# Optimization experiments

Hardware: AMD Instinct MI355X
Metric: run time of the kernel (lower is better)

## Reference

```python
import jax, jax.numpy as jnp
from jax import lax
import numpy as np

N = 4096      # nnodes
D = 64        # embed_dim
R = 128       # nodes per region
G = N // R    # 32 regions (contiguous blocks)
BIG = 1e9     # 'no edge' cost (scipy MST treats zero-similarity entries as absent edges)


def setup_inputs() -> dict:
    key = jax.random.key(0)
    emb = jax.random.normal(key, (N, D), dtype=jnp.float32) * 0.05  # nn.Embedding weight (xavier-like scale)
    region_id = jnp.arange(N) // R
    inter_mask = (region_id[:, None] != region_id[None, :]).astype(jnp.float32)  # block off-diagonal buffer
    return {"emb_weight": emb, "inter_mask": inter_mask, "inter_budget": 1024}


def _prim_forest_mask(W):
    """Prim's algorithm on dense cost matrix W [R,R] (BIG = missing edge).
    Returns symmetric 0/1 minimum-spanning-FOREST edge mask, matching
    scipy.sparse.csgraph.minimum_spanning_tree on the same graph (weights distinct)."""
    r = W.shape[0]

    def step(carry, _):
        in_tree, key_, parent, mask = carry
        km = jnp.where(in_tree, BIG, key_)
        u = jnp.argmin(km)                          # cheapest node to attach
        valid = (km[u] < BIG * 0.5).astype(W.dtype)  # BIG key => start new component, no edge
        p = parent[u]
        mask = mask.at[u, p].add(valid)
        mask = mask.at[p, u].add(valid)
        in_tree = in_tree.at[u].set(True)
        wu = W[u]
        improve = (~in_tree) & (wu < key_)
        key_ = jnp.where(improve, wu, key_)
        parent = jnp.where(improve, u, parent)
        return (in_tree, key_, parent, mask), None

    in_tree0 = jnp.zeros(r, dtype=bool).at[0].set(True)
    key0 = W[0]
    parent0 = jnp.zeros(r, dtype=jnp.int32)
    mask0 = jnp.zeros_like(W)
    (_, _, _, mask), _ = lax.scan(step, (in_tree0, key0, parent0, mask0), None, length=r - 1)
    return (mask > 0).astype(W.dtype)


def reference(emb_weight, inter_mask, inter_budget):
    # adj_dense = relu(tanh(E E^T))  [N,N]
    adj = jax.nn.relu(jnp.tanh(emb_weight @ emb_weight.T))
    adj_ng = lax.stop_gradient(adj)  # torch: MST input is .detach(); top-k indices carry no grad

    # ---- intra: per-region MST (max spanning forest of similarity == min SF of -sim) ----
    blocks = adj_ng.reshape(G, R, G, R)[jnp.arange(G), :, jnp.arange(G), :]  # [G,R,R] diagonal blocks
    eye = jnp.eye(R, dtype=bool)
    W = jnp.where((blocks > 0) & ~eye, -blocks, BIG)  # zero similarity => no edge (scipy semantics)
    intra_blocks = jax.vmap(_prim_forest_mask)(W)     # [G,R,R]
    idx = jnp.arange(N).reshape(G, R)
    intra = jnp.zeros((N, N), adj.dtype).at[idx[:, :, None], idx[:, None, :]].set(intra_blocks)
    intra = intra * (1.0 - jnp.eye(N, dtype=adj.dtype))  # fill_diagonal_(0)

    # ---- inter: global top-k over upper-triangular masked similarities ----
    flat = jnp.triu(adj_ng * inter_mask, k=1).reshape(-1)  # [N*N]
    k = int(inter_budget)  # == min(budget, nnz(inter_mask)//2); budget is smaller by construction
    _, top_idx = lax.top_k(flat, k)
    inter_sel = jnp.zeros(N * N, adj.dtype).at[top_idx].set(1.0).reshape(N, N)
    inter_sel = inter_sel + inter_sel.T

    final_mask = ((intra + inter_sel) > 0).astype(adj.dtype)
    return adj * final_mask
```

## Files before the change

kernel.cpp:

```cpp
#include <hip/hip_runtime.h>

#define NN 4096
#define DD 64
#define RR 128
#define GG 32
constexpr unsigned BIGH = 0xCE6E6B28u;
constexpr unsigned FLOOR_KEY = 0x3D000000u;
constexpr int FLOORB = 0x3D0;
constexpr int NBINS  = 64;
constexpr unsigned POISON = 0xAAAAAAAAu;

constexpr int WS_FH   = 0;
constexpr int WS_ECNT = 2051;
constexpr int WS_CCNT = 2052;
constexpr int WS_MIJ  = 2112;
constexpr int WS_MV   = WS_MIJ + 4096;
constexpr int WS_EI   = WS_MV + 4096;
constexpr int WS_EJ   = WS_EI + 8192;
constexpr int WS_EV   = WS_EJ + 8192;
constexpr int WS_CK   = WS_EV + 8192;
constexpr int WS_CI   = WS_CK + 8192;
constexpr int EDGE_CAP = 8192;
constexpr int CAND_CAP = 8192;

__device__ __forceinline__ void pair_decode(int p, int& gi, int& gj) {
  gi = 0;
  int rem = p;
  while (rem >= GG - 1 - gi) { rem -= GG - 1 - gi; ++gi; }
  gj = gi + 1 + rem;
}

__device__ __forceinline__ void scan_bins(const unsigned* __restrict__ ws, unsigned k,
                                          unsigned* shm ,
                                          unsigned& tlo, unsigned& thi, unsigned& rem) {
  const int t = threadIdx.x;
  if (t < NBINS) shm[t] = ws[WS_FH + FLOORB + t] - POISON;
  __syncthreads();
  if (t == 0) {
    unsigned cum = 0;
    int fb = FLOORB;
    unsigned r = 0;
    for (int b = NBINS - 1; b >= 0; --b) {
      unsigned c = shm[b];
      if (cum + c >= k) { fb = FLOORB + b; r = k - cum; break; }
      cum += c;
    }
    shm[64] = ((unsigned)fb) << 20;
    shm[65] = ((unsigned)(fb + 1)) << 20;
    shm[66] = r;
  }
  __syncthreads();
  tlo = shm[64];
  thi = shm[65];
  rem = shm[66];
}

__global__ __launch_bounds__(256) void gemm_adj_kernel(const float* __restrict__ E,
                                                       float* __restrict__ adj,
                                                       unsigned* __restrict__ ws) {
  const int ti = blockIdx.y, tj = blockIdx.x;
  const bool rdiag = (ti >> 1) == (tj >> 1);
  if (tj < ti && !rdiag) return;
  const bool cross = (tj >> 1) > (ti >> 1);

  __shared__ float4 As4[64 * 16];
  __shared__ float4 Bs4[64 * 16];
  __shared__ unsigned h[NBINS];
  const float4* E4 = (const float4*)E;
  const int bi = ti * 64, bj = tj * 64;
  const int tid = threadIdx.x;

  if (tid < NBINS) h[tid] = 0;

#pragma unroll
  for (int it = 0; it < 4; ++it) {
    int row = (tid >> 4) + it * 16;
    int g = tid & 15;
    int sw = g ^ ((row >> 2) & 7);
    As4[row * 16 + sw] = E4[(bi + row) * 16 + g];
    Bs4[row * 16 + sw] = E4[(bj + row) * 16 + g];
  }
  __syncthreads();

  const int i0 = (tid >> 4) * 4;
  const int j0 = (tid & 15) * 4;
  const int sa = (i0 >> 2) & 7;
  const int sb = (j0 >> 2) & 7;
  float acc[4][4] = {};
#pragma unroll 2
  for (int k4 = 0; k4 < 16; ++k4) {
    float4 av[4], bv[4];
#pragma unroll
    for (int r = 0; r < 4; ++r) av[r] = As4[(i0 + r) * 16 + (k4 ^ sa)];
#pragma unroll
    for (int c = 0; c < 4; ++c) bv[c] = Bs4[(j0 + c) * 16 + (k4 ^ sb)];
#pragma unroll
    for (int r = 0; r < 4; ++r)
#pragma unroll
      for (int c = 0; c < 4; ++c) {
        acc[r][c] += av[r].x * bv[c].x;
        acc[r][c] += av[r].y * bv[c].y;
        acc[r][c] += av[r].z * bv[c].z;
        acc[r][c] += av[r].w * bv[c].w;
      }
  }
#pragma unroll
  for (int r = 0; r < 4; ++r) {
    float4 o;
    float* p = &o.x;
#pragma unroll
    for (int c = 0; c < 4; ++c) {
      float t = tanhf(acc[r][c]);
      p[c] = t > 0.f ? t : 0.f;
    }
    *(float4*)(adj + (size_t)(bi + i0 + r) * NN + bj + j0) = o;
    if (cross) {
#pragma unroll
      for (int c = 0; c < 4; ++c) {
        unsigned key = __float_as_uint(p[c]);
        if (key >= FLOOR_KEY) atomicAdd(&h[(key >> 20) - FLOORB], 1u);
      }
    }
  }
  if (cross) {
    __syncthreads();
    if (tid < NBINS) {
      unsigned c = h[tid];
      if (c) atomicAdd(&ws[WS_FH + FLOORB + tid], c);
    }
  }
}

template <int CTRL>
__device__ __forceinline__ unsigned dpp_umin(unsigned v) {
  unsigned o = (unsigned)__builtin_amdgcn_update_dpp((int)v, (int)v, CTRL, 0xF, 0xF, false);
  return o < v ? o : v;
}
__device__ __forceinline__ unsigned xfneg(float a) {
  return ~__float_as_uint(a) & 0x7FFFFFFFu;
}

__global__ __launch_bounds__(64) void mst_kernel(const float* __restrict__ adj, unsigned* ws) {
  __shared__ float W[RR * RR];
  const int g = blockIdx.x, l = threadIdx.x, base = g * RR;
  float4* W4 = (float4*)W;
  const float4* A4 = (const float4*)adj;

#pragma unroll
  for (int n = 0; n < 64; ++n) {
    int f = l + 64 * n;
    W4[f] = A4[(size_t)(base + (f >> 5)) * (NN / 4) + (base >> 2) + (f & 31)];
  }
  __syncthreads();

  const int n0 = l, n1 = l + 64;
  float a0 = W[n0], a1 = W[n1];
  unsigned key0 = (n0 != 0 && a0 > 0.f) ? xfneg(a0) : BIGH;
  unsigned key1 = (a1 > 0.f) ? xfneg(a1) : BIGH;
  bool in0 = (l == 0), in1 = false;
  int par0 = 0, par1 = 0;
  unsigned e0ij = 0xFFFFFFFFu, e1ij = 0xFFFFFFFFu;
  float e0v = 0.f, e1v = 0.f;

  for (int it = 0; it < RR - 1; ++it) {
    const unsigned kA = in0 ? BIGH : key0;
    const unsigned kB = in1 ? BIGH : key1;
    unsigned km = kA < kB ? kA : kB;
    km = dpp_umin<0xB1>(km);
    km = dpp_umin<0x4E>(km);
    km = dpp_umin<0x141>(km);
    km = dpp_umin<0x140>(km);
    const unsigned r0 = (unsigned)__builtin_amdgcn_readlane((int)km, 15);
    const unsigned r1 = (unsigned)__builtin_amdgcn_readlane((int)km, 31);
    const unsigned r2 = (unsigned)__builtin_amdgcn_readlane((int)km, 47);
    const unsigned r3 = (unsigned)__builtin_amdgcn_readlane((int)km, 63);
    const unsigned ma = r0 < r1 ? r0 : r1;
    const unsigned mb = r2 < r3 ? r2 : r3;
    const unsigned m = ma < mb ? ma : mb;

    const unsigned long long b0 = __ballot(kA == m);
    const unsigned long long b1 = __ballot(kB == m);
    const int u = b0 ? (__ffsll((unsigned long long)b0) - 1)
                     : (64 + __ffsll((unsigned long long)b1) - 1);

    const int p0 = __builtin_amdgcn_readlane(par0, u & 63);
    const int p1 = __builtin_amdgcn_readlane(par1, u & 63);
    const int par = (u >> 6) ? p1 : p0;
    unsigned pij = 0xFFFFFFFFu;
    float pv = 0.f;
    if ((int)m >= 0) {
      pij = ((unsigned)(base + u) << 12) | (unsigned)(base + par);
      pv = __uint_as_float(~m & 0x7FFFFFFFu);
    }
    const bool mine = (l == (it & 63));
    if (it & 64) { if (mine) { e1ij = pij; e1v = pv; } }
    else         { if (mine) { e0ij = pij; e0v = pv; } }

    in0 = in0 || (u == n0);
    in1 = in1 || (u == n1);
    float w0v = W[u * RR + n0];
    float w1v = W[u * RR + n1];
    unsigned w0 = (w0v > 0.f && n0 != u) ? xfneg(w0v) : BIGH;
    unsigned w1 = (w1v > 0.f && n1 != u) ? xfneg(w1v) : BIGH;
    if (!in0 && w0 < key0) { key0 = w0; par0 = u; }
    if (!in1 && w1 < key1) { key1 = w1; par1 = u; }
  }
  ws[WS_MIJ + base + l] = e0ij;
  ws[WS_MIJ + base + 64 + l] = e1ij;
  ((float*)(ws + WS_MV))[base + l] = e0v;
  ((float*)(ws + WS_MV))[base + 64 + l] = e1v;
}

__global__ __launch_bounds__(256) void collect_kernel(const float* __restrict__ adj,
                                                      unsigned* ws, const int* budget) {
  __shared__ unsigned shm[67];
  unsigned tlo, thi, rem;
  scan_bins(ws, (unsigned)budget[0], shm, tlo, thi, rem);
  (void)rem;
  int gi, gj;
  pair_decode(blockIdx.x, gi, gj);
  const float4* a4 = (const float4*)adj;
  for (int e = threadIdx.x; e < RR * 32; e += 256) {
    int r = e >> 5, c4 = e & 31;
    float4 v = a4[(size_t)(gi * RR + r) * (NN / 4) + gj * 32 + c4];
    float comp[4] = {v.x, v.y, v.z, v.w};
#pragma unroll
    for (int c = 0; c < 4; ++c) {
      float x = comp[c];
      if (!(x > 0.f)) continue;
      unsigned key = __float_as_uint(x);
      if (key < tlo) continue;
      int i = gi * RR + r, j = gj * RR + c4 * 4 + c;
      if (key >= thi) {
        unsigned slot = atomicAdd(ws + WS_ECNT, 1u) - POISON;
        if (slot < EDGE_CAP) {
          ((int*)(ws + WS_EI))[slot] = i;
          ((int*)(ws + WS_EJ))[slot] = j;
          ((float*)(ws + WS_EV))[slot] = x;
        }
      } else {
        unsigned s2 = atomicAdd(ws + WS_CCNT, 1u) - POISON;
        if (s2 < CAND_CAP) {
          ws[WS_CK + s2] = key;
          ws[WS_CI + s2] = (unsigned)((i << 12) | j);
        }
      }
    }
  }
}

__global__ __launch_bounds__(1024) void topk_kernel(unsigned* ws, const int* budget) {
  __shared__ unsigned long long s[CAND_CAP];
  __shared__ unsigned shm[67];
  unsigned tlo, thi, rem;
  scan_bins(ws, (unsigned)budget[0], shm, tlo, thi, rem);
  (void)tlo; (void)thi;
  const int t = threadIdx.x;
  unsigned n = ws[WS_CCNT] - POISON;
  if (n > CAND_CAP) n = CAND_CAP;
  unsigned m = 2;
  while (m < n) m <<= 1;
  for (int i = t; i < (int)m; i += 1024) {
    unsigned long long v = 0ull;
    if (i < (int)n)
      v = ((unsigned long long)ws[WS_CK + i] << 32) |
          (unsigned long long)(0x00FFFFFFu - ws[WS_CI + i]);
    s[i] = v;
  }
  for (unsigned size = 2; size <= m; size <<= 1)
    for (unsigned stride = size >> 1; stride; stride >>= 1) {
      __syncthreads();
      for (unsigned i = t; i < m / 2; i += 1024) {
        unsigned lo = ((i & ~(stride - 1)) << 1) | (i & (stride - 1));
        unsigned hi = lo | stride;
        bool up = ((lo & size) == 0);
        unsigned long long a = s[lo], b = s[hi];
        if ((a > b) == up) { s[lo] = b; s[hi] = a; }
      }
    }
  __syncthreads();
  for (unsigned p = t; p < rem; p += 1024) {
    unsigned long long v = s[m - 1 - p];
    if (v == 0ull) continue;
    unsigned key = (unsigned)(v >> 32);
    unsigned idx = 0x00FFFFFFu - (unsigned)(v & 0xFFFFFFFFull);
    unsigned slot = atomicAdd(ws + WS_ECNT, 1u) - POISON;
    if (slot < EDGE_CAP) {
      ((int*)(ws + WS_EI))[slot] = (int)(idx >> 12);
      ((int*)(ws + WS_EJ))[slot] = (int)(idx & 4095u);
      ((float*)(ws + WS_EV))[slot] = __uint_as_float(key);
    }
  }
}

__global__ __launch_bounds__(256) void zero_scatter_kernel(const unsigned* __restrict__ ws,
                                                           float* __restrict__ out) {
  const int bid = blockIdx.x;
  const int r0 = bid * 16;
  float4* out4 = (float4*)(out + (size_t)r0 * NN);
  const float4 z = make_float4(0.f, 0.f, 0.f, 0.f);
  for (int e = threadIdx.x; e < 16 * (NN / 4); e += 256) out4[e] = z;
  __syncthreads();
  unsigned cnt = ws[WS_ECNT] - POISON;
  if (cnt > EDGE_CAP) cnt = EDGE_CAP;
  const int tot = 4096 + (int)cnt;
  for (int e = threadIdx.x; e < tot; e += 256) {
    int i, j;
    float v;
    if (e < 4096) {
      unsigned pij = ws[WS_MIJ + e];
      if (pij == 0xFFFFFFFFu) continue;
      i = (int)(pij >> 12);
      j = (int)(pij & 4095u);
      v = ((const float*)(ws + WS_MV))[e];
    } else {
      int q = e - 4096;
      i = ((const int*)(ws + WS_EI))[q];
      j = ((const int*)(ws + WS_EJ))[q];
      v = ((const float*)(ws + WS_EV))[q];
    }
    if ((i >> 4) == bid) out[(size_t)i * NN + j] = v;
    if ((j >> 4) == bid) out[(size_t)j * NN + i] = v;
  }
}

extern "C" void kernel_launch(void* const* d_in, const int* in_sizes, int n_in,
                              void* d_out, int out_size, void* d_ws, size_t ws_size,
                              hipStream_t stream) {
  const float* E      = (const float*)d_in[0];
  const int*   budget = (const int*)d_in[2];
  float*    adj = (float*)d_out;
  unsigned* ws  = (unsigned*)d_ws;

  gemm_adj_kernel<<<dim3(NN / 64, NN / 64), 256, 0, stream>>>(E, adj, ws);
  mst_kernel<<<GG, 64, 0, stream>>>(adj, ws);
  collect_kernel<<<GG * (GG - 1) / 2, 256, 0, stream>>>(adj, ws, budget);
  topk_kernel<<<1, 1024, 0, stream>>>(ws, budget);
  zero_scatter_kernel<<<256, 256, 0, stream>>>(ws, adj);
}
```

Before: 251.5 us.

## Move adj to workspace, zero output inside MST loop, fuse scatter into topk

The dense adjacency now lives in workspace instead of the output buffer. The latency-bound MST blocks zero the 64MB output while they iterate, hiding the zeroing behind the serial Prim loop. The final scatter is folded into the single-block topk kernel, which removes one launch and a full zeroing pass. The cost is that the MST blocks take on heavy store traffic, that only 32 blocks do the zeroing, and that the scatter now runs on a single block.

```diff
diff --git a/kernel.cpp b/kernel.cpp
--- a/kernel.cpp
+++ b/kernel.cpp
@@ -20,6 +20,7 @@
 constexpr int WS_EV   = WS_EJ + 8192;
 constexpr int WS_CK   = WS_EV + 8192;
 constexpr int WS_CI   = WS_CK + 8192;
+constexpr size_t ADJ_OFF = 8u * 1024u * 1024u;
 constexpr int EDGE_CAP = 8192;
 constexpr int CAND_CAP = 8192;
 
@@ -140,11 +141,15 @@
   return ~__float_as_uint(a) & 0x7FFFFFFFu;
 }
 
-__global__ __launch_bounds__(64) void mst_kernel(const float* __restrict__ adj, unsigned* ws) {
+__global__ __launch_bounds__(64) void mst_kernel(const float* __restrict__ adj,
+                                                 unsigned* __restrict__ ws,
+                                                 float* __restrict__ out) {
   __shared__ float W[RR * RR];
   const int g = blockIdx.x, l = threadIdx.x, base = g * RR;
   float4* W4 = (float4*)W;
   const float4* A4 = (const float4*)adj;
+  float4* z4 = (float4*)out + (size_t)g * (NN * (size_t)NN / 4 / GG);
+  const float4 zz = make_float4(0.f, 0.f, 0.f, 0.f);
 
 #pragma unroll
   for (int n = 0; n < 64; ++n) {
@@ -163,6 +168,9 @@
   float e0v = 0.f, e1v = 0.f;
 
   for (int it = 0; it < RR - 1; ++it) {
+#pragma unroll
+    for (int s = 0; s < 16; ++s) z4[(it * 16 + s) * 64 + l] = zz;
+
     const unsigned kA = in0 ? BIGH : key0;
     const unsigned kB = in1 ? BIGH : key1;
     unsigned km = kA < kB ? kA : kB;
@@ -205,6 +213,9 @@
     if (!in0 && w0 < key0) { key0 = w0; par0 = u; }
     if (!in1 && w1 < key1) { key1 = w1; par1 = u; }
   }
+#pragma unroll
+  for (int s = 0; s < 16; ++s) z4[130048 + s * 64 + l] = zz;
+
   ws[WS_MIJ + base + l] = e0ij;
   ws[WS_MIJ + base + 64 + l] = e1ij;
   ((float*)(ws + WS_MV))[base + l] = e0v;
@@ -249,7 +260,8 @@
   }
 }
 
-__global__ __launch_bounds__(1024) void topk_kernel(unsigned* ws, const int* budget) {
+__global__ __launch_bounds__(1024) void topk_scatter_kernel(unsigned* ws, const int* budget,
+                                                            float* __restrict__ out) {
   __shared__ unsigned long long s[CAND_CAP];
   __shared__ unsigned shm[67];
   unsigned tlo, thi, rem;
@@ -291,20 +303,11 @@
       ((float*)(ws + WS_EV))[slot] = __uint_as_float(key);
     }
   }
-}
-
-__global__ __launch_bounds__(256) void zero_scatter_kernel(const unsigned* __restrict__ ws,
-                                                           float* __restrict__ out) {
-  const int bid = blockIdx.x;
-  const int r0 = bid * 16;
-  float4* out4 = (float4*)(out + (size_t)r0 * NN);
-  const float4 z = make_float4(0.f, 0.f, 0.f, 0.f);
-  for (int e = threadIdx.x; e < 16 * (NN / 4); e += 256) out4[e] = z;
-  __syncthreads();
-  unsigned cnt = ws[WS_ECNT] - POISON;
+  __syncthreads();
+  unsigned cnt = atomicAdd(ws + WS_ECNT, 0u) - POISON;
   if (cnt > EDGE_CAP) cnt = EDGE_CAP;
   const int tot = 4096 + (int)cnt;
-  for (int e = threadIdx.x; e < tot; e += 256) {
+  for (int e = t; e < tot; e += 1024) {
     int i, j;
     float v;
     if (e < 4096) {
@@ -319,8 +322,8 @@
       j = ((const int*)(ws + WS_EJ))[q];
       v = ((const float*)(ws + WS_EV))[q];
     }
-    if ((i >> 4) == bid) out[(size_t)i * NN + j] = v;
-    if ((j >> 4) == bid) out[(size_t)j * NN + i] = v;
+    out[(size_t)i * NN + j] = v;
+    out[(size_t)j * NN + i] = v;
   }
 }
 
@@ -329,12 +332,12 @@
                               hipStream_t stream) {
   const float* E      = (const float*)d_in[0];
   const int*   budget = (const int*)d_in[2];
-  float*    adj = (float*)d_out;
   unsigned* ws  = (unsigned*)d_ws;
+  float*    adj = (float*)(ws + ADJ_OFF);
+  float*    out = (float*)d_out;
 
   gemm_adj_kernel<<<dim3(NN / 64, NN / 64), 256, 0, stream>>>(E, adj, ws);
-  mst_kernel<<<GG, 64, 0, stream>>>(adj, ws);
+  mst_kernel<<<GG, 64, 0, stream>>>(adj, ws, out);
   collect_kernel<<<GG * (GG - 1) / 2, 256, 0, stream>>>(adj, ws, budget);
-  topk_kernel<<<1, 1024, 0, stream>>>(ws, budget);
-  zero_scatter_kernel<<<256, 256, 0, stream>>>(ws, adj);
-}
+  topk_scatter_kernel<<<1, 1024, 0, stream>>>(ws, budget, out);
+}
```

Result: no change. 256.4 us (+1.9%).
